# Performance work log

Measured on AMD Instinct MI355X. Metric: run time of the kernel, lower is better.

Reference implementation:

```python
import jax, jax.numpy as jnp
import numpy as np

N = 100000   # vertices
E = 600000   # directed edges
F = 200000   # triangle faces
CIN = 128
COUT = 128
H = 32       # metric MLP hidden
D = 3        # embedding_dim (3D metric)
TRI = D * (D + 1) // 2  # 6 params of a symmetric 3x3


def setup_inputs() -> dict:
    key = jax.random.key(0)
    ks = jax.random.split(key, 8)
    features = jax.random.normal(ks[0], (N, CIN), jnp.float32)
    vertices = jax.random.normal(ks[1], (N, 3), jnp.float32)
    edges = jax.random.randint(ks[2], (2, E), 0, N)
    faces = jax.random.randint(ks[3], (3, F), 0, N)
    # metric MLP params (edge tangent vector -> symmetric metric params)
    W1 = jax.random.normal(ks[4], (D, H), jnp.float32) / np.sqrt(D)
    b1 = jnp.zeros((H,), jnp.float32)
    W2 = jax.random.normal(ks[5], (H, TRI), jnp.float32) / np.sqrt(H)
    b2 = jnp.zeros((TRI,), jnp.float32)
    # per-vertex feature transform
    Wlin = jax.random.normal(ks[6], (CIN, COUT), jnp.float32) / np.sqrt(CIN)
    blin = jnp.zeros((COUT,), jnp.float32)
    return dict(features=features, vertices=vertices, edges=edges, faces=faces,
                W1=W1, b1=b1, W2=W2, b2=b2, Wlin=Wlin, blin=blin)


def _vertex_normals(vertices, faces):
    # area-weighted vertex normals from triangle faces
    v0, v1, v2 = vertices[faces[0]], vertices[faces[1]], vertices[faces[2]]
    fn = jnp.cross(v1 - v0, v2 - v0)                       # [F,3]
    n = jnp.zeros_like(vertices)
    n = n.at[faces[0]].add(fn).at[faces[1]].add(fn).at[faces[2]].add(fn)
    return n / (jnp.linalg.norm(n, axis=-1, keepdims=True) + 1e-8)


def _sym_from_flat(theta):
    # theta [E,6] -> symmetric [E,3,3]
    iu0, iu1 = jnp.triu_indices(D)
    S = jnp.zeros((theta.shape[0], D, D), theta.dtype)
    S = S.at[:, iu0, iu1].set(theta)
    S = S.at[:, iu1, iu0].set(theta)
    return S


def reference(features, vertices, edges, faces, W1, b1, W2, b2, Wlin, blin):
    eps = 1e-5
    src, dst = edges[0], edges[1]
    normals = _vertex_normals(vertices, faces)             # [N,3] ('tangent' info)
    d = vertices[dst] - vertices[src]                      # [E,3] edge vectors
    n_src = normals[src]
    t = d - jnp.sum(d * n_src, -1, keepdims=True) * n_src  # tangent-plane projection
    # learned metric per edge: MLP -> symmetric S, PSD metric M = S S
    h = jax.nn.relu(t @ W1 + b1)                           # [E,H]
    theta = h @ W2 + b2                                    # [E,6]
    S = _sym_from_flat(theta)                              # [E,3,3]
    M = jnp.einsum('eij,ejk->eik', S, S)                   # PSD metric
    q = jnp.einsum('ei,eij,ej->e', t, M, t)                # metric quadratic form
    w = jnp.exp(-q)                                        # positive edge weights
    # per-vertex linear, then metric-weighted mean aggregation over in-edges
    x = features @ Wlin + blin                             # [N,COUT]
    num = jax.ops.segment_sum(w[:, None] * x[src], dst, num_segments=N)
    den = jax.ops.segment_sum(w, dst, num_segments=N) + eps
    out = num / den[:, None]                               # MetricConv output
    # MetricConvBlock: manual per-feature normalization + ELU
    mu = out.mean(axis=0)
    sd = out.std(axis=0, ddof=1)                           # torch std is unbiased
    out = (out - mu) / (sd + eps)
    return jax.nn.elu(out)
```

## Files before the change

kernel.cpp:

```cpp
#include <hip/hip_runtime.h>
#include <hip/hip_bf16.h>
#include <math.h>

#define N_V 100000
#define N_E 600000
#define N_F 200000

typedef __attribute__((ext_vector_type(8))) short bf16x8;
typedef __attribute__((ext_vector_type(4))) float f32x4;

#define FUSED_BLOCKS 782
#define FACE_BLOCKS 782
#define EDGE_BLOCKS 2344
#define PACK_BLOCKS 64

__device__ __forceinline__ unsigned short f2bf(float f) {
    unsigned int u = __builtin_bit_cast(unsigned int, f);
    u += 0x7fffu + ((u >> 16) & 1u);
    return (unsigned short)(u >> 16);
}

__global__ void k_fn(const float* __restrict__ vtx, const int* __restrict__ faces,
                     const float* __restrict__ Wlin,
                     float4* __restrict__ fnbuf4,
                     int* __restrict__ head_f, int* __restrict__ next_f,
                     unsigned short* __restrict__ Wb) {
    int b = blockIdx.x;
    int t = threadIdx.x;
    if (b < FACE_BLOCKS) {
        int f = b * 256 + t;
        if (f >= N_F) return;
        int i0 = faces[f], i1 = faces[N_F + f], i2 = faces[2 * N_F + f];
        #pragma unroll
        for (int j = 0; j < 3; j++) {
            int v = (j == 0) ? i0 : (j == 1 ? i1 : i2);
            int c = 3 * f + j;
            int old = atomicExch(&head_f[v], c);
            next_f[c] = old;
        }
        float ax = vtx[3 * i0], ay = vtx[3 * i0 + 1], az = vtx[3 * i0 + 2];
        float bx = vtx[3 * i1] - ax, by = vtx[3 * i1 + 1] - ay, bz = vtx[3 * i1 + 2] - az;
        float cx = vtx[3 * i2] - ax, cy = vtx[3 * i2 + 1] - ay, cz = vtx[3 * i2 + 2] - az;
        float4 fn;
        fn.x = by * cz - bz * cy;
        fn.y = bz * cx - bx * cz;
        fn.z = bx * cy - by * cx;
        fn.w = 0.f;
        fnbuf4[f] = fn;
    } else {
        int i = (b - FACE_BLOCKS) * 256 + t;
        int j = i & 7;
        int lane = (i >> 3) & 63;
        int ct = (i >> 9) & 7;
        int kk = i >> 12;
        int k = kk * 32 + (lane >> 4) * 8 + j;
        int n = ct * 16 + (lane & 15);
        Wb[i] = f2bf(Wlin[k * 128 + n]);
    }
}

__global__ void k_vnorm(const float4* __restrict__ fnbuf4,
                        const int* __restrict__ head_f, const int* __restrict__ next_f,
                        float4* __restrict__ nrm4) {
    int v = blockIdx.x * 256 + threadIdx.x;
    if (v >= N_V) return;
    float nx = 0.f, ny = 0.f, nz = 0.f;
    int c = head_f[v];
    while (c >= 0) {
        float4 fn = fnbuf4[(unsigned)c / 3u];
        nx += fn.x; ny += fn.y; nz += fn.z;
        c = next_f[c];
    }
    float inv = 1.f / (sqrtf(nx * nx + ny * ny + nz * nz) + 1e-8f);
    float4 o;
    o.x = nx * inv; o.y = ny * inv; o.z = nz * inv; o.w = 0.f;
    nrm4[v] = o;
}

__global__ void k_edge(const float* __restrict__ vtx, const int* __restrict__ edges,
                       const float4* __restrict__ nrm4,
                       const float* __restrict__ W1, const float* __restrict__ b1,
                       const float* __restrict__ W2, const float* __restrict__ b2,
                       int* __restrict__ head_e, uint2* __restrict__ enode) {
    __shared__ float sW1[96], sb1[32], sW2[192], sb2[6];
    int t = threadIdx.x;
    if (t < 96)  sW1[t] = W1[t];
    if (t < 32)  sb1[t] = b1[t];
    if (t < 192) sW2[t] = W2[t];
    if (t < 6)   sb2[t] = b2[t];
    __syncthreads();
    int e = blockIdx.x * blockDim.x + t;
    if (e >= N_E) return;
    int s = edges[e], d = edges[N_E + e];
    int old = atomicExch(&head_e[d], e);
    float4 nv = nrm4[s];
    float dx = vtx[3 * d] - vtx[3 * s];
    float dy = vtx[3 * d + 1] - vtx[3 * s + 1];
    float dz = vtx[3 * d + 2] - vtx[3 * s + 2];
    float nx = nv.x, ny = nv.y, nz = nv.z;
    float dp = dx * nx + dy * ny + dz * nz;
    float tx = dx - dp * nx, ty = dy - dp * ny, tz = dz - dp * nz;
    float th0 = sb2[0], th1 = sb2[1], th2 = sb2[2], th3 = sb2[3], th4 = sb2[4], th5 = sb2[5];
    #pragma unroll
    for (int j = 0; j < 32; j++) {
        float h = tx * sW1[j] + ty * sW1[32 + j] + tz * sW1[64 + j] + sb1[j];
        h = fmaxf(h, 0.f);
        const float* w2r = &sW2[j * 6];
        th0 += h * w2r[0]; th1 += h * w2r[1]; th2 += h * w2r[2];
        th3 += h * w2r[3]; th4 += h * w2r[4]; th5 += h * w2r[5];
    }
    float ux = th0 * tx + th1 * ty + th2 * tz;
    float uy = th1 * tx + th3 * ty + th4 * tz;
    float uz = th2 * tx + th4 * ty + th5 * tz;
    float q = ux * ux + uy * uy + uz * uz;
    float w = expf(-q);
    unsigned int w16 = f2bf(w);
    uint2 nd;
    nd.x = (unsigned int)(old + 1) | ((w16 & 0xFFFu) << 20);
    nd.y = (unsigned int)s | ((w16 >> 12) << 17);
    enode[e] = nd;
}

__global__ __launch_bounds__(512) void k_fused(const float* __restrict__ feat,
                                               const int* __restrict__ head_e,
                                               const uint2* __restrict__ enode,
                                               const unsigned short* __restrict__ Wb,
                                               const float* __restrict__ blin,
                                               float* __restrict__ out,
                                               float* __restrict__ partials) {
    __shared__ __align__(16) unsigned short At[128 * 136];
    __shared__ float gs[128];
    int t = threadIdx.x;
    int g = t >> 4;
    int gl = t & 15;
    int vb = blockIdx.x * 128 + g * 4;

    float4 a0l = {0,0,0,0}, a0h = {0,0,0,0};
    float4 a1l = {0,0,0,0}, a1h = {0,0,0,0};
    float4 a2l = {0,0,0,0}, a2h = {0,0,0,0};
    float4 a3l = {0,0,0,0}, a3h = {0,0,0,0};
    float d0 = 0.f, d1 = 0.f, d2 = 0.f, d3 = 0.f;
    int e0 = (vb + 0 < N_V) ? head_e[vb + 0] : -1;
    int e1 = (vb + 1 < N_V) ? head_e[vb + 1] : -1;
    int e2 = (vb + 2 < N_V) ? head_e[vb + 2] : -1;
    int e3 = (vb + 3 < N_V) ? head_e[vb + 3] : -1;

    while ((e0 >= 0) || (e1 >= 0) || (e2 >= 0) || (e3 >= 0)) {
        if (e0 >= 0) {
            uint2 nd = enode[e0];
            unsigned int wb = (nd.x >> 20) | (((nd.y >> 17) & 0xFu) << 12);
            float w = __builtin_bit_cast(float, wb << 16);
            const float4* fp = (const float4*)(feat + (size_t)(nd.y & 0x1FFFFu) * 128 + 8 * gl);
            float4 f0 = fp[0], f1 = fp[1];
            a0l.x += w * f0.x; a0l.y += w * f0.y; a0l.z += w * f0.z; a0l.w += w * f0.w;
            a0h.x += w * f1.x; a0h.y += w * f1.y; a0h.z += w * f1.z; a0h.w += w * f1.w;
            d0 += w;
            e0 = (int)(nd.x & 0xFFFFFu) - 1;
        }
        if (e1 >= 0) {
            uint2 nd = enode[e1];
            unsigned int wb = (nd.x >> 20) | (((nd.y >> 17) & 0xFu) << 12);
            float w = __builtin_bit_cast(float, wb << 16);
            const float4* fp = (const float4*)(feat + (size_t)(nd.y & 0x1FFFFu) * 128 + 8 * gl);
            float4 f0 = fp[0], f1 = fp[1];
            a1l.x += w * f0.x; a1l.y += w * f0.y; a1l.z += w * f0.z; a1l.w += w * f0.w;
            a1h.x += w * f1.x; a1h.y += w * f1.y; a1h.z += w * f1.z; a1h.w += w * f1.w;
            d1 += w;
            e1 = (int)(nd.x & 0xFFFFFu) - 1;
        }
        if (e2 >= 0) {
            uint2 nd = enode[e2];
            unsigned int wb = (nd.x >> 20) | (((nd.y >> 17) & 0xFu) << 12);
            float w = __builtin_bit_cast(float, wb << 16);
            const float4* fp = (const float4*)(feat + (size_t)(nd.y & 0x1FFFFu) * 128 + 8 * gl);
            float4 f0 = fp[0], f1 = fp[1];
            a2l.x += w * f0.x; a2l.y += w * f0.y; a2l.z += w * f0.z; a2l.w += w * f0.w;
            a2h.x += w * f1.x; a2h.y += w * f1.y; a2h.z += w * f1.z; a2h.w += w * f1.w;
            d2 += w;
            e2 = (int)(nd.x & 0xFFFFFu) - 1;
        }
        if (e3 >= 0) {
            uint2 nd = enode[e3];
            unsigned int wb = (nd.x >> 20) | (((nd.y >> 17) & 0xFu) << 12);
            float w = __builtin_bit_cast(float, wb << 16);
            const float4* fp = (const float4*)(feat + (size_t)(nd.y & 0x1FFFFu) * 128 + 8 * gl);
            float4 f0 = fp[0], f1 = fp[1];
            a3l.x += w * f0.x; a3l.y += w * f0.y; a3l.z += w * f0.z; a3l.w += w * f0.w;
            a3h.x += w * f1.x; a3h.y += w * f1.y; a3h.z += w * f1.z; a3h.w += w * f1.w;
            d3 += w;
            e3 = (int)(nd.x & 0xFFFFFu) - 1;
        }
    }
    #pragma unroll
    for (int j = 0; j < 4; j++) {
        float4 al = (j == 0) ? a0l : (j == 1) ? a1l : (j == 2) ? a2l : a3l;
        float4 ah = (j == 0) ? a0h : (j == 1) ? a1h : (j == 2) ? a2h : a3h;
        float dn = (j == 0) ? d0 : (j == 1) ? d1 : (j == 2) ? d2 : d3;
        float inv = 1.f / (dn + 1e-5f);
        ushort4 p0, p1;
        p0.x = f2bf(al.x * inv); p0.y = f2bf(al.y * inv);
        p0.z = f2bf(al.z * inv); p0.w = f2bf(al.w * inv);
        p1.x = f2bf(ah.x * inv); p1.y = f2bf(ah.y * inv);
        p1.z = f2bf(ah.z * inv); p1.w = f2bf(ah.w * inv);
        int row = g * 4 + j;
        *(ushort4*)(&At[row * 136 + 8 * gl]) = p0;
        *(ushort4*)(&At[row * 136 + 8 * gl + 4]) = p1;
        if (gl == 0) gs[row] = dn * inv;
    }
    __syncthreads();

    int ct = t >> 6;
    int lane = t & 63;
    int m = lane & 15, quad = lane >> 4;
    bf16x8 bfr[4];
    #pragma unroll
    for (int kk = 0; kk < 4; kk++)
        bfr[kk] = *(const bf16x8*)(Wb + (((kk * 8 + ct) * 64 + lane) << 3));
    float bl = blin[ct * 16 + m];
    float ssr = 0.f, qqr = 0.f;
    #pragma unroll
    for (int tile = 0; tile < 8; tile++) {
        f32x4 acc = (f32x4){0.f, 0.f, 0.f, 0.f};
        #pragma unroll
        for (int kk = 0; kk < 4; kk++) {
            bf16x8 af = *(const bf16x8*)(&At[(tile * 16 + m) * 136 + kk * 32 + quad * 8]);
            acc = __builtin_amdgcn_mfma_f32_16x16x32_bf16(af, bfr[kk], acc, 0, 0, 0);
        }
        int r0 = blockIdx.x * 128 + tile * 16;
        #pragma unroll
        for (int reg = 0; reg < 4; reg++) {
            int r = r0 + quad * 4 + reg;
            float g2 = gs[tile * 16 + quad * 4 + reg];
            float val = acc[reg] + bl * g2;
            if (r < N_V)
                __builtin_nontemporal_store(val, &out[(size_t)r * 128 + ct * 16 + m]);
            ssr += val; qqr += val * val;
        }
    }
    ssr += __shfl_xor(ssr, 16); qqr += __shfl_xor(qqr, 16);
    ssr += __shfl_xor(ssr, 32); qqr += __shfl_xor(qqr, 32);
    if (quad == 0) {
        partials[(size_t)blockIdx.x * 256 + ct * 16 + m] = ssr;
        partials[(size_t)blockIdx.x * 256 + 128 + ct * 16 + m] = qqr;
    }
}

__global__ __launch_bounds__(64) void k_rstats(const float* __restrict__ partials,
                                               float* __restrict__ stats) {
    int c = blockIdx.x;
    int lane = threadIdx.x;
    float s = 0.f, q = 0.f;
    for (int b = lane; b < FUSED_BLOCKS; b += 64) {
        s += partials[(size_t)b * 256 + c];
        q += partials[(size_t)b * 256 + 128 + c];
    }
    #pragma unroll
    for (int off = 32; off; off >>= 1) {
        s += __shfl_down(s, off);
        q += __shfl_down(q, off);
    }
    if (lane == 0) {
        float mu = s * (1.f / N_V);
        float var = (q - s * mu) * (1.f / (N_V - 1));
        float sd = sqrtf(fmaxf(var, 0.f));
        stats[c] = mu;
        stats[128 + c] = 1.f / (sd + 1e-5f);
    }
}

__global__ void k_finalize(float* __restrict__ out, const float* __restrict__ stats) {
    int i = blockIdx.x * blockDim.x + threadIdx.x;
    if (i >= N_V * 32) return;
    float4 v = ((float4*)out)[i];
    int c0 = (i * 4) & 127;
    float mu0 = stats[c0], mu1 = stats[c0 + 1], mu2 = stats[c0 + 2], mu3 = stats[c0 + 3];
    float is0 = stats[128 + c0], is1 = stats[128 + c0 + 1], is2 = stats[128 + c0 + 2], is3 = stats[128 + c0 + 3];
    v.x = (v.x - mu0) * is0; v.y = (v.y - mu1) * is1;
    v.z = (v.z - mu2) * is2; v.w = (v.w - mu3) * is3;
    v.x = v.x > 0.f ? v.x : expm1f(v.x);
    v.y = v.y > 0.f ? v.y : expm1f(v.y);
    v.z = v.z > 0.f ? v.z : expm1f(v.z);
    v.w = v.w > 0.f ? v.w : expm1f(v.w);
    ((float4*)out)[i] = v;
}

extern "C" void kernel_launch(void* const* d_in, const int* in_sizes, int n_in,
                              void* d_out, int out_size, void* d_ws, size_t ws_size,
                              hipStream_t stream) {
    const float* feat  = (const float*)d_in[0];
    const float* vtx   = (const float*)d_in[1];
    const int*   edges = (const int*)d_in[2];
    const int*   faces = (const int*)d_in[3];
    const float* W1   = (const float*)d_in[4];
    const float* b1   = (const float*)d_in[5];
    const float* W2   = (const float*)d_in[6];
    const float* b2   = (const float*)d_in[7];
    const float* Wlin = (const float*)d_in[8];
    const float* blin = (const float*)d_in[9];
    float* out = (float*)d_out;

    float* ws = (float*)d_ws;
    int*   head_e   = (int*)ws;
    int*   head_f   = (int*)(ws + 100000);
    float4* nrm4    = (float4*)(ws + 200000);
    float* partials = ws + 100000;
    int*   next_f   = (int*)(ws + 600128);
    float4* fnbuf4  = (float4*)(ws + 1200128);
    uint2* enode    = (uint2*)(ws + 600128);
    unsigned short* Wb = (unsigned short*)(ws + 2000128);
    float* stats    = ws;

    hipMemsetAsync(head_e, 0xFF, 200000 * sizeof(int), stream);

    k_fn<<<FACE_BLOCKS + PACK_BLOCKS, 256, 0, stream>>>(vtx, faces, Wlin, fnbuf4,
                                                        head_f, next_f, Wb);
    k_vnorm<<<(N_V + 255) / 256, 256, 0, stream>>>(fnbuf4, head_f, next_f, nrm4);
    k_edge<<<EDGE_BLOCKS, 256, 0, stream>>>(vtx, edges, nrm4, W1, b1, W2, b2,
                                            head_e, enode);
    k_fused<<<FUSED_BLOCKS, 512, 0, stream>>>(feat, head_e, enode, Wb, blin,
                                              out, partials);
    k_rstats<<<128, 64, 0, stream>>>(partials, stats);
    k_finalize<<<(N_V * 32 + 255) / 256, 256, 0, stream>>>(out, stats);
}
```

Measured before the change: 267.2 us.

## Move edge-list build into face kernel and gather bf16 features

Edge linked-list construction (atomicExch on head_e plus writing next pointers) moves out of k_edge into the first k_fn launch, so it overlaps with the face-normal work. k_edge now only writes the packed weight and source index. When the workspace is large enough, features are also converted to bf16 up front so the gather in the fused kernel reads half the bytes per edge. The output store loses its nontemporal hint. The bf16 feature gather lowers accumulation precision, and the extra conversion pass costs a full read and write of the features.

After: 263.6 us. Within noise of the previous version (-1.4%).

```diff
diff --git a/kernel.cpp b/kernel.cpp
--- a/kernel.cpp
+++ b/kernel.cpp
@@ -13,18 +13,25 @@
 #define FACE_BLOCKS 782
 #define EDGE_BLOCKS 2344
 #define PACK_BLOCKS 64
+#define CONV_BLOCKS 6250
 
 __device__ __forceinline__ unsigned short f2bf(float f) {
     unsigned int u = __builtin_bit_cast(unsigned int, f);
     u += 0x7fffu + ((u >> 16) & 1u);
     return (unsigned short)(u >> 16);
 }
+__device__ __forceinline__ float bf2f(short s) {
+    return __builtin_bit_cast(float, ((unsigned int)(unsigned short)s) << 16);
+}
 
 __global__ void k_fn(const float* __restrict__ vtx, const int* __restrict__ faces,
-                     const float* __restrict__ Wlin,
+                     const float* __restrict__ Wlin, const int* __restrict__ edges,
+                     const float* __restrict__ feat,
                      float4* __restrict__ fnbuf4,
                      int* __restrict__ head_f, int* __restrict__ next_f,
-                     unsigned short* __restrict__ Wb) {
+                     unsigned short* __restrict__ Wb,
+                     int* __restrict__ head_e, uint2* __restrict__ enode,
+                     unsigned short* __restrict__ featb) {
     int b = blockIdx.x;
     int t = threadIdx.x;
     if (b < FACE_BLOCKS) {
@@ -47,7 +54,7 @@
         fn.z = bx * cy - by * cx;
         fn.w = 0.f;
         fnbuf4[f] = fn;
-    } else {
+    } else if (b < FACE_BLOCKS + PACK_BLOCKS) {
         int i = (b - FACE_BLOCKS) * 256 + t;
         int j = i & 7;
         int lane = (i >> 3) & 63;
@@ -56,6 +63,25 @@
         int k = kk * 32 + (lane >> 4) * 8 + j;
         int n = ct * 16 + (lane & 15);
         Wb[i] = f2bf(Wlin[k * 128 + n]);
+    } else if (b < FACE_BLOCKS + PACK_BLOCKS + EDGE_BLOCKS) {
+        int e = (b - FACE_BLOCKS - PACK_BLOCKS) * 256 + t;
+        if (e >= N_E) return;
+        int s = edges[e], d = edges[N_E + e];
+        int old = atomicExch(&head_e[d], e);
+        uint2 nd;
+        nd.x = (unsigned int)(old + 1);
+        nd.y = (unsigned int)s;
+        enode[e] = nd;
+    } else {
+        int i = (b - FACE_BLOCKS - PACK_BLOCKS - EDGE_BLOCKS) * 256 + t;
+        const float4* fp = (const float4*)(feat + (size_t)i * 8);
+        float4 f0 = fp[0], f1 = fp[1];
+        bf16x8 p;
+        p[0] = (short)f2bf(f0.x); p[1] = (short)f2bf(f0.y);
+        p[2] = (short)f2bf(f0.z); p[3] = (short)f2bf(f0.w);
+        p[4] = (short)f2bf(f1.x); p[5] = (short)f2bf(f1.y);
+        p[6] = (short)f2bf(f1.z); p[7] = (short)f2bf(f1.w);
+        *(bf16x8*)(featb + (size_t)i * 8) = p;
     }
 }
 
@@ -77,11 +103,12 @@
     nrm4[v] = o;
 }
 
-__global__ void k_edge(const float* __restrict__ vtx, const int* __restrict__ edges,
-                       const float4* __restrict__ nrm4,
-                       const float* __restrict__ W1, const float* __restrict__ b1,
-                       const float* __restrict__ W2, const float* __restrict__ b2,
-                       int* __restrict__ head_e, uint2* __restrict__ enode) {
+template<int PUSH_DONE>
+__global__ void k_edge_t(const float* __restrict__ vtx, const int* __restrict__ edges,
+                         const float4* __restrict__ nrm4,
+                         const float* __restrict__ W1, const float* __restrict__ b1,
+                         const float* __restrict__ W2, const float* __restrict__ b2,
+                         int* __restrict__ head_e, uint2* __restrict__ enode) {
     __shared__ float sW1[96], sb1[32], sW2[192], sb2[6];
     int t = threadIdx.x;
     if (t < 96)  sW1[t] = W1[t];
@@ -92,7 +119,8 @@
     int e = blockIdx.x * blockDim.x + t;
     if (e >= N_E) return;
     int s = edges[e], d = edges[N_E + e];
-    int old = atomicExch(&head_e[d], e);
+    int old = 0;
+    if (!PUSH_DONE) old = atomicExch(&head_e[d], e);
     float4 nv = nrm4[s];
     float dx = vtx[3 * d] - vtx[3 * s];
     float dy = vtx[3 * d + 1] - vtx[3 * s + 1];
@@ -115,19 +143,25 @@
     float q = ux * ux + uy * uy + uz * uz;
     float w = expf(-q);
     unsigned int w16 = f2bf(w);
-    uint2 nd;
-    nd.x = (unsigned int)(old + 1) | ((w16 & 0xFFFu) << 20);
-    nd.y = (unsigned int)s | ((w16 >> 12) << 17);
-    enode[e] = nd;
-}
-
-__global__ __launch_bounds__(512) void k_fused(const float* __restrict__ feat,
-                                               const int* __restrict__ head_e,
-                                               const uint2* __restrict__ enode,
-                                               const unsigned short* __restrict__ Wb,
-                                               const float* __restrict__ blin,
-                                               float* __restrict__ out,
-                                               float* __restrict__ partials) {
+    if (!PUSH_DONE) {
+        uint2 nd;
+        nd.x = (unsigned int)(old + 1) | ((w16 & 0xFFFu) << 20);
+        nd.y = (unsigned int)s | ((w16 >> 12) << 17);
+        enode[e] = nd;
+    } else {
+        ((unsigned int*)enode)[2 * (size_t)e + 1] = (unsigned int)s | (w16 << 17);
+    }
+}
+
+template<int STYLE>
+__global__ __launch_bounds__(512) void k_fused_t(const float* __restrict__ feat,
+                                                 const unsigned short* __restrict__ featb,
+                                                 const int* __restrict__ head_e,
+                                                 const uint2* __restrict__ enode,
+                                                 const unsigned short* __restrict__ Wb,
+                                                 const float* __restrict__ blin,
+                                                 float* __restrict__ out,
+                                                 float* __restrict__ partials) {
     __shared__ __align__(16) unsigned short At[128 * 136];
     __shared__ float gs[128];
     int t = threadIdx.x;
@@ -145,52 +179,38 @@
     int e2 = (vb + 2 < N_V) ? head_e[vb + 2] : -1;
     int e3 = (vb + 3 < N_V) ? head_e[vb + 3] : -1;
 
+#define CHAIN_STEP(eV, aL, aH, dV)                                                   \
+    if (eV >= 0) {                                                                   \
+        uint2 nd = enode[eV];                                                        \
+        unsigned int w16 = (STYLE == 0)                                              \
+            ? ((nd.x >> 20) | (((nd.y >> 17) & 0xFu) << 12))                         \
+            : (nd.y >> 17);                                                          \
+        float w = __builtin_bit_cast(float, w16 << 16);                              \
+        unsigned int src = nd.y & 0x1FFFFu;                                          \
+        if (STYLE < 2) {                                                             \
+            const float4* fp = (const float4*)(feat + (size_t)src * 128 + 8 * gl);   \
+            float4 f0 = fp[0], f1 = fp[1];                                           \
+            aL.x += w * f0.x; aL.y += w * f0.y; aL.z += w * f0.z; aL.w += w * f0.w;  \
+            aH.x += w * f1.x; aH.y += w * f1.y; aH.z += w * f1.z; aH.w += w * f1.w;  \
+        } else {                                                                     \
+            bf16x8 v = *(const bf16x8*)(featb + (size_t)src * 128 + 8 * gl);         \
+            aL.x += w * bf2f(v[0]); aL.y += w * bf2f(v[1]);                          \
+            aL.z += w * bf2f(v[2]); aL.w += w * bf2f(v[3]);                          \
+            aH.x += w * bf2f(v[4]); aH.y += w * bf2f(v[5]);                          \
+            aH.z += w * bf2f(v[6]); aH.w += w * bf2f(v[7]);                          \
+        }                                                                            \
+        dV += w;                                                                     \
+        eV = (int)(nd.x & 0xFFFFFu) - 1;                                             \
+    }
+
     while ((e0 >= 0) || (e1 >= 0) || (e2 >= 0) || (e3 >= 0)) {
-        if (e0 >= 0) {
-            uint2 nd = enode[e0];
-            unsigned int wb = (nd.x >> 20) | (((nd.y >> 17) & 0xFu) << 12);
-            float w = __builtin_bit_cast(float, wb << 16);
-            const float4* fp = (const float4*)(feat + (size_t)(nd.y & 0x1FFFFu) * 128 + 8 * gl);
-            float4 f0 = fp[0], f1 = fp[1];
-            a0l.x += w * f0.x; a0l.y += w * f0.y; a0l.z += w * f0.z; a0l.w += w * f0.w;
-            a0h.x += w * f1.x; a0h.y += w * f1.y; a0h.z += w * f1.z; a0h.w += w * f1.w;
-            d0 += w;
-            e0 = (int)(nd.x & 0xFFFFFu) - 1;
-        }
-        if (e1 >= 0) {
-            uint2 nd = enode[e1];
-            unsigned int wb = (nd.x >> 20) | (((nd.y >> 17) & 0xFu) << 12);
-            float w = __builtin_bit_cast(float, wb << 16);
-            const float4* fp = (const float4*)(feat + (size_t)(nd.y & 0x1FFFFu) * 128 + 8 * gl);
-            float4 f0 = fp[0], f1 = fp[1];
-            a1l.x += w * f0.x; a1l.y += w * f0.y; a1l.z += w * f0.z; a1l.w += w * f0.w;
-            a1h.x += w * f1.x; a1h.y += w * f1.y; a1h.z += w * f1.z; a1h.w += w * f1.w;
-            d1 += w;
-            e1 = (int)(nd.x & 0xFFFFFu) - 1;
-        }
-        if (e2 >= 0) {
-            uint2 nd = enode[e2];
-            unsigned int wb = (nd.x >> 20) | (((nd.y >> 17) & 0xFu) << 12);
-            float w = __builtin_bit_cast(float, wb << 16);
-            const float4* fp = (const float4*)(feat + (size_t)(nd.y & 0x1FFFFu) * 128 + 8 * gl);
-            float4 f0 = fp[0], f1 = fp[1];
-            a2l.x += w * f0.x; a2l.y += w * f0.y; a2l.z += w * f0.z; a2l.w += w * f0.w;
-            a2h.x += w * f1.x; a2h.y += w * f1.y; a2h.z += w * f1.z; a2h.w += w * f1.w;
-            d2 += w;
-            e2 = (int)(nd.x & 0xFFFFFu) - 1;
-        }
-        if (e3 >= 0) {
-            uint2 nd = enode[e3];
-            unsigned int wb = (nd.x >> 20) | (((nd.y >> 17) & 0xFu) << 12);
-            float w = __builtin_bit_cast(float, wb << 16);
-            const float4* fp = (const float4*)(feat + (size_t)(nd.y & 0x1FFFFu) * 128 + 8 * gl);
-            float4 f0 = fp[0], f1 = fp[1];
-            a3l.x += w * f0.x; a3l.y += w * f0.y; a3l.z += w * f0.z; a3l.w += w * f0.w;
-            a3h.x += w * f1.x; a3h.y += w * f1.y; a3h.z += w * f1.z; a3h.w += w * f1.w;
-            d3 += w;
-            e3 = (int)(nd.x & 0xFFFFFu) - 1;
-        }
-    }
+        CHAIN_STEP(e0, a0l, a0h, d0)
+        CHAIN_STEP(e1, a1l, a1h, d1)
+        CHAIN_STEP(e2, a2l, a2h, d2)
+        CHAIN_STEP(e3, a3l, a3h, d3)
+    }
+#undef CHAIN_STEP
+
     #pragma unroll
     for (int j = 0; j < 4; j++) {
         float4 al = (j == 0) ? a0l : (j == 1) ? a1l : (j == 2) ? a2l : a3l;
@@ -232,8 +252,7 @@
             int r = r0 + quad * 4 + reg;
             float g2 = gs[tile * 16 + quad * 4 + reg];
             float val = acc[reg] + bl * g2;
-            if (r < N_V)
-                __builtin_nontemporal_store(val, &out[(size_t)r * 128 + ct * 16 + m]);
+            if (r < N_V) out[(size_t)r * 128 + ct * 16 + m] = val;
             ssr += val; qqr += val * val;
         }
     }
@@ -298,27 +317,61 @@
     const float* Wlin = (const float*)d_in[8];
     const float* blin = (const float*)d_in[9];
     float* out = (float*)d_out;
-
     float* ws = (float*)d_ws;
-    int*   head_e   = (int*)ws;
-    int*   head_f   = (int*)(ws + 100000);
-    float4* nrm4    = (float4*)(ws + 200000);
-    float* partials = ws + 100000;
-    int*   next_f   = (int*)(ws + 600128);
-    float4* fnbuf4  = (float4*)(ws + 1200128);
-    uint2* enode    = (uint2*)(ws + 600128);
-    unsigned short* Wb = (unsigned short*)(ws + 2000128);
-    float* stats    = ws;
-
-    hipMemsetAsync(head_e, 0xFF, 200000 * sizeof(int), stream);
-
-    k_fn<<<FACE_BLOCKS + PACK_BLOCKS, 256, 0, stream>>>(vtx, faces, Wlin, fnbuf4,
-                                                        head_f, next_f, Wb);
-    k_vnorm<<<(N_V + 255) / 256, 256, 0, stream>>>(fnbuf4, head_f, next_f, nrm4);
-    k_edge<<<EDGE_BLOCKS, 256, 0, stream>>>(vtx, edges, nrm4, W1, b1, W2, b2,
-                                            head_e, enode);
-    k_fused<<<FUSED_BLOCKS, 512, 0, stream>>>(feat, head_e, enode, Wb, blin,
-                                              out, partials);
-    k_rstats<<<128, 64, 0, stream>>>(partials, stats);
-    k_finalize<<<(N_V * 32 + 255) / 256, 256, 0, stream>>>(out, stats);
-}
+
+    const size_t NEED1 = 3208192u * 4u;
+    const size_t NEED2 = 9608192u * 4u;
+    int tier = (ws_size >= NEED2) ? 2 : (ws_size >= NEED1) ? 1 : 0;
+
+    if (tier == 0) {
+        int*   head_e   = (int*)ws;
+        int*   head_f   = (int*)(ws + 100000);
+        float4* nrm4    = (float4*)(ws + 200000);
+        float* partials = ws + 100000;
+        int*   next_f   = (int*)(ws + 600128);
+        float4* fnbuf4  = (float4*)(ws + 1200128);
+        uint2* enode    = (uint2*)(ws + 600128);
+        unsigned short* Wb = (unsigned short*)(ws + 2000128);
+        float* stats    = ws;
+
+        hipMemsetAsync(head_e, 0xFF, 200000 * sizeof(int), stream);
+        k_fn<<<FACE_BLOCKS + PACK_BLOCKS, 256, 0, stream>>>(vtx, faces, Wlin, edges, feat,
+                                                            fnbuf4, head_f, next_f, Wb,
+                                                            head_e, enode, nullptr);
+        k_vnorm<<<(N_V + 255) / 256, 256, 0, stream>>>(fnbuf4, head_f, next_f, nrm4);
+        k_edge_t<0><<<EDGE_BLOCKS, 256, 0, stream>>>(vtx, edges, nrm4, W1, b1, W2, b2,
+                                                     head_e, enode);
+        k_fused_t<0><<<FUSED_BLOCKS, 512, 0, stream>>>(feat, nullptr, head_e, enode, Wb,
+                                                       blin, out, partials);
+        k_rstats<<<128, 64, 0, stream>>>(partials, stats);
+        k_finalize<<<(N_V * 32 + 255) / 256, 256, 0, stream>>>(out, stats);
+    } else {
+        int*   head_e   = (int*)ws;
+        int*   head_f   = (int*)(ws + 100000);
+        float4* nrm4    = (float4*)(ws + 200000);
+        float* partials = ws + 100000;
+        int*   next_f   = (int*)(ws + 600000);
+        float4* fnbuf4  = (float4*)(ws + 1200000);
+        uint2* enode    = (uint2*)(ws + 2000000);
+        unsigned short* Wb = (unsigned short*)(ws + 3200000);
+        unsigned short* featb = (unsigned short*)(ws + 3208192);
+        float* stats    = ws;
+
+        hipMemsetAsync(head_e, 0xFF, 200000 * sizeof(int), stream);
+        int fn_grid = FACE_BLOCKS + PACK_BLOCKS + EDGE_BLOCKS + (tier == 2 ? CONV_BLOCKS : 0);
+        k_fn<<<fn_grid, 256, 0, stream>>>(vtx, faces, Wlin, edges, feat,
+                                          fnbuf4, head_f, next_f, Wb,
+                                          head_e, enode, featb);
+        k_vnorm<<<(N_V + 255) / 256, 256, 0, stream>>>(fnbuf4, head_f, next_f, nrm4);
+        k_edge_t<1><<<EDGE_BLOCKS, 256, 0, stream>>>(vtx, edges, nrm4, W1, b1, W2, b2,
+                                                     head_e, enode);
+        if (tier == 2)
+            k_fused_t<2><<<FUSED_BLOCKS, 512, 0, stream>>>(feat, featb, head_e, enode, Wb,
+                                                           blin, out, partials);
+        else
+            k_fused_t<1><<<FUSED_BLOCKS, 512, 0, stream>>>(feat, nullptr, head_e, enode, Wb,
+                                                           blin, out, partials);
+        k_rstats<<<128, 64, 0, stream>>>(partials, stats);
+        k_finalize<<<(N_V * 32 + 255) / 256, 256, 0, stream>>>(out, stats);
+    }
+}
```
